# Performance work log

Measured on AMD Instinct MI355X. Metric: run time of the kernel, lower is better.

## Reference

```python
import jax, jax.numpy as jnp
import numpy as np

N, E, G = 100000, 1600000, 1000
F_IN, H, C = 16, 64, 2
EPS = 1e-5


def setup_inputs() -> dict:
    key = jax.random.key(0)
    ks = jax.random.split(key, 8)

    def lin(k, i, o):
        return (jax.random.normal(k, (i, o), jnp.float32) / np.float32(np.sqrt(i)))

    return {
        "x": jax.random.normal(ks[0], (N, F_IN), jnp.float32),
        "edge_index": jax.random.randint(ks[1], (2, E), 0, N),
        "batch": jnp.sort(jax.random.randint(ks[2], (N,), 0, G)),
        # GraphNorm params: weight=1, bias=0, mean_scale(alpha)=1 (PyG init)
        "gn0_w": jnp.ones(F_IN, jnp.float32), "gn0_b": jnp.zeros(F_IN, jnp.float32), "gn0_a": jnp.ones(F_IN, jnp.float32),
        "W1": lin(ks[3], F_IN, H), "b1": jnp.zeros(H, jnp.float32),
        "gn1_w": jnp.ones(H, jnp.float32), "gn1_b": jnp.zeros(H, jnp.float32), "gn1_a": jnp.ones(H, jnp.float32),
        "W2": lin(ks[4], H, H), "b2": jnp.zeros(H, jnp.float32),
        "gn2_w": jnp.ones(H, jnp.float32), "gn2_b": jnp.zeros(H, jnp.float32), "gn2_a": jnp.ones(H, jnp.float32),
        "W3": lin(ks[5], H, H), "b3": jnp.zeros(H, jnp.float32),
        "Wd": lin(ks[6], H, H), "bd": jnp.zeros(H, jnp.float32),
        "Wo": lin(ks[7], H, C), "bo": jnp.zeros(C, jnp.float32),
    }


def _graph_norm(x, batch, w, b, a):
    counts = jnp.maximum(jax.ops.segment_sum(jnp.ones(x.shape[0], x.dtype), batch, G), 1.0)[:, None]
    mean = jax.ops.segment_sum(x, batch, G) / counts          # [G, F]
    out = x - a * mean[batch]
    var = jax.ops.segment_sum(out * out, batch, G) / counts   # [G, F]
    return w * (out * jax.lax.rsqrt(var + EPS)[batch]) + b


def _gcn_conv(x, W, b, src, dst):
    # PyG GCNConv: D^{-1/2}(A+I)D^{-1/2} X W + b, deg includes self-loop
    h = x @ W                                                  # [N, out]
    deg = jax.ops.segment_sum(jnp.ones(src.shape[0], x.dtype), dst, N) + 1.0
    dinv = jax.lax.rsqrt(deg)
    msg = h[src] * (dinv[src] * dinv[dst])[:, None]            # [E, out]
    agg = jax.ops.segment_sum(msg, dst, N) + h / deg[:, None]  # self-loop term: 1/deg
    return agg + b


def reference(x, edge_index, batch, gn0_w, gn0_b, gn0_a, W1, b1,
              gn1_w, gn1_b, gn1_a, W2, b2, gn2_w, gn2_b, gn2_a,
              W3, b3, Wd, bd, Wo, bo):
    src, dst = edge_index[0], edge_index[1]
    x = _graph_norm(x, batch, gn0_w, gn0_b, gn0_a)
    x = jax.nn.relu(_gcn_conv(x, W1, b1, src, dst))
    x = _graph_norm(x, batch, gn1_w, gn1_b, gn1_a)
    x = jax.nn.relu(_gcn_conv(x, W2, b2, src, dst))
    x = _graph_norm(x, batch, gn2_w, gn2_b, gn2_a)
    x = jax.nn.relu(_gcn_conv(x, W3, b3, src, dst))
    counts = jnp.maximum(jax.ops.segment_sum(jnp.ones(N, x.dtype), batch, G), 1.0)
    pooled = jax.ops.segment_sum(x, batch, G) / counts[:, None]  # global_mean_pool [G, H]
    # dropout p=0.5 is identity in eval mode
    h = jax.nn.relu(pooled @ Wd + bd)
    logits = h @ Wo + bo
    return jax.nn.softmax(logits, axis=1)
```

## Files before the change

kernel.cpp:

```cpp
#include <hip/hip_runtime.h>
#include <hip/hip_fp16.h>
#include <math.h>

#define NB_NODES 100000
#define NB_EDGES 1600000
#define NB_GRAPHS 1000
#define CAP 232
#define NBLK1 400
#define CHUNK 4000
#define NBUCK 391
#define BCAP 4608
constexpr float GN_EPS = 1e-5f;

__global__ __launch_bounds__(256) void k1_hist(const int* __restrict__ dst,
    int* __restrict__ hist, const int* __restrict__ batch, int* __restrict__ gstart) {
    __shared__ int h[NBUCK];
    int tid = threadIdx.x;
    for (int i = tid; i < NBUCK; i += 256) h[i] = 0;
    if (blockIdx.x < 4) {
        int g = blockIdx.x * 256 + tid;
        if (g <= NB_GRAPHS) {
            int lo = 0, hi = NB_NODES;
            while (lo < hi) {
                int mid = (lo + hi) >> 1;
                if (batch[mid] < g) lo = mid + 1; else hi = mid;
            }
            gstart[g] = lo;
        }
    }
    __syncthreads();
    int base = blockIdx.x * CHUNK;
    for (int i = tid; i < CHUNK; i += 256) atomicAdd(&h[dst[base + i] >> 8], 1);
    __syncthreads();
    for (int i = tid; i < NBUCK; i += 256) hist[blockIdx.x * NBUCK + i] = h[i];
}

__global__ __launch_bounds__(512) void k2a_scan(int* __restrict__ hist,
                                                int* __restrict__ total) {
    __shared__ int s[512];
    int b = blockIdx.x;
    int tid = threadIdx.x;
    int v = (tid < NBLK1) ? hist[tid * NBUCK + b] : 0;
    s[tid] = v;
    __syncthreads();
    for (int o = 1; o < 512; o <<= 1) {
        int t = (tid >= o) ? s[tid - o] : 0;
        __syncthreads();
        s[tid] += t;
        __syncthreads();
    }
    if (tid < NBLK1) hist[tid * NBUCK + b] = s[tid] - v;
    if (tid == 511) total[b] = s[511];
}

__global__ __launch_bounds__(256) void k3_scatter(const int* __restrict__ ei,
    const int* __restrict__ hist, const int* __restrict__ total,
    unsigned int* __restrict__ ebuf) {
    __shared__ int cur[NBUCK];
    __shared__ int sc[256];
    int tid = threadIdx.x;
    int e0 = 2 * tid, e1 = 2 * tid + 1;
    int v0 = (e0 < NBUCK) ? total[e0] : 0;
    int v1 = (e1 < NBUCK) ? total[e1] : 0;
    int own = v0 + v1;
    sc[tid] = own;
    __syncthreads();
    for (int o = 1; o < 256; o <<= 1) {
        int t = (tid >= o) ? sc[tid - o] : 0;
        __syncthreads();
        sc[tid] += t;
        __syncthreads();
    }
    int pre = sc[tid] - own;
    if (e0 < NBUCK) cur[e0] = pre + hist[blockIdx.x * NBUCK + e0];
    if (e1 < NBUCK) cur[e1] = pre + v0 + hist[blockIdx.x * NBUCK + e1];
    __syncthreads();
    int eb = blockIdx.x * CHUNK;
    for (int i = tid; i < CHUNK; i += 256) {
        int e = eb + i;
        int sidx = ei[e];
        int d = ei[NB_EDGES + e];
        int pos = atomicAdd(&cur[d >> 8], 1);
        ebuf[pos] = (unsigned int)sidx | ((unsigned int)(d & 255) << 24);
    }
}

__global__ __launch_bounds__(256) void k4_fine(const unsigned int* __restrict__ ebuf,
    const int* __restrict__ total, int* __restrict__ csr_src, int* __restrict__ rowptr,
    float* __restrict__ dinv) {
    __shared__ int arena[2 * BCAP + 768];
    unsigned int* epk = (unsigned int*)arena;
    int* outb  = arena + BCAP;
    int* cnt   = arena + 2 * BCAP;
    int* sbuf  = arena + 2 * BCAP + 256;
    int* cur2  = arena + 2 * BCAP + 512;
    int* bases = arena + 2 * BCAP;
    int b = blockIdx.x;
    int tid = threadIdx.x;
    int e0 = 2 * tid, e1 = 2 * tid + 1;
    int v0 = (e0 < NBUCK) ? total[e0] : 0;
    int v1 = (e1 < NBUCK) ? total[e1] : 0;
    int own = v0 + v1;
    cur2[tid] = own;
    __syncthreads();
    for (int o = 1; o < 256; o <<= 1) {
        int t = (tid >= o) ? cur2[tid - o] : 0;
        __syncthreads();
        cur2[tid] += t;
        __syncthreads();
    }
    int pre = cur2[tid] - own;
    if (e0 < NBUCK) bases[e0] = pre;
    if (e1 < NBUCK) bases[e1] = pre + v0;
    if (tid == 0) bases[NBUCK] = NB_EDGES;
    __syncthreads();
    int eb = bases[b], ee = bases[b + 1];
    __syncthreads();
    int m = ee - eb;
    if (m > BCAP) m = BCAP;
    for (int i = tid; i < m; i += 256) epk[i] = ebuf[eb + i];
    cnt[tid] = 0;
    __syncthreads();
    for (int i = tid; i < m; i += 256) atomicAdd(&cnt[epk[i] >> 24], 1);
    __syncthreads();
    int c = cnt[tid];
    sbuf[tid] = c;
    __syncthreads();
    for (int o = 1; o < 256; o <<= 1) {
        int t = (tid >= o) ? sbuf[tid - o] : 0;
        __syncthreads();
        sbuf[tid] += t;
        __syncthreads();
    }
    int off = sbuf[tid] - c;
    cur2[tid] = off;
    __syncthreads();
    for (int i = tid; i < m; i += 256) {
        unsigned int p = epk[i];
        int r = atomicAdd(&cur2[p >> 24], 1);
        outb[r] = (int)(p & 0x00FFFFFFu);
    }
    __syncthreads();
    for (int i = tid; i < m; i += 256) csr_src[eb + i] = outb[i];
    int node = b * 256 + tid;
    if (node < NB_NODES) {
        rowptr[node] = eb + off;
        dinv[node] = rsqrtf((float)(c + 1));
    }
    if (b == 0 && tid == 0) rowptr[NB_NODES] = NB_EDGES;
}

union HU {
    uint4 u;
    __half2 h[4];
};

__device__ __forceinline__ void pkacc(__half2* a, uint4 v) {
    HU x; x.u = v;
    a[0] = __hadd2(a[0], x.h[0]);
    a[1] = __hadd2(a[1], x.h[1]);
    a[2] = __hadd2(a[2], x.h[2]);
    a[3] = __hadd2(a[3], x.h[3]);
}

__device__ __forceinline__ __half2 shxor_h2(__half2 v, int m) {
    union { __half2 h; int i; } u;
    u.h = v;
    u.i = __shfl_xor(u.i, m, 64);
    return u.h;
}

__global__ __launch_bounds__(256) void aggregate_h_k(const __half* __restrict__ hs,
    const int* __restrict__ rowptr, const int* __restrict__ csr_src,
    const float* __restrict__ dinv, const float* __restrict__ bias,
    __half* __restrict__ out) {
    const uint4* hsv = (const uint4*)hs;
    int wv = blockIdx.x * 4 + (threadIdx.x >> 6);
    int lane = threadIdx.x & 63;
    int f8 = lane & 7;
    int e8 = lane >> 3;
    int n0 = __builtin_amdgcn_readfirstlane(wv * 4);
    int r0 = rowptr[n0], r1 = rowptr[n0 + 1], r2 = rowptr[n0 + 2];
    int r3 = rowptr[n0 + 3], r4 = rowptr[n0 + 4];
    int d0 = r1 - r0, d1 = r2 - r1, d2 = r3 - r2, d3 = r4 - r3;
    const uint4 Z = {0u, 0u, 0u, 0u};
    int idx0 = (lane < d0) ? csr_src[r0 + lane] : -1;
    int idx1 = (lane < d1) ? csr_src[r1 + lane] : -1;
    int idx2 = (lane < d2) ? csr_src[r2 + lane] : -1;
    int idx3 = (lane < d3) ? csr_src[r3 + lane] : -1;
    uint4 self = Z;
    if (e8 < 4) self = hsv[(size_t)(n0 + e8) * 8 + f8];
    uint4 gA[8];
#pragma unroll
    for (int b = 0; b < 4; b++) {
        int u = __shfl(idx0, b * 8 + e8, 64);
        gA[b] = Z;
        if (u >= 0) gA[b] = hsv[(size_t)u * 8 + f8];
        int v = __shfl(idx1, b * 8 + e8, 64);
        gA[4 + b] = Z;
        if (v >= 0) gA[4 + b] = hsv[(size_t)v * 8 + f8];
    }
    __half2 acc0[4], acc1[4], acc2[4], acc3[4];
    __half2 z2{__half(0.f), __half(0.f)};
    acc0[0] = acc0[1] = acc0[2] = acc0[3] = z2;
    acc1[0] = acc1[1] = acc1[2] = acc1[3] = z2;
    acc2[0] = acc2[1] = acc2[2] = acc2[3] = z2;
    acc3[0] = acc3[1] = acc3[2] = acc3[3] = z2;
    if (e8 == 0) pkacc(acc0, self);
    if (e8 == 1) pkacc(acc1, self);
    if (e8 == 2) pkacc(acc2, self);
    if (e8 == 3) pkacc(acc3, self);
    uint4 gB[8];
#pragma unroll
    for (int b = 0; b < 4; b++) {
        int u = __shfl(idx2, b * 8 + e8, 64);
        gB[b] = Z;
        if (u >= 0) gB[b] = hsv[(size_t)u * 8 + f8];
        int v = __shfl(idx3, b * 8 + e8, 64);
        gB[4 + b] = Z;
        if (v >= 0) gB[4 + b] = hsv[(size_t)v * 8 + f8];
    }
#pragma unroll
    for (int b = 0; b < 4; b++) { pkacc(acc0, gA[b]); pkacc(acc1, gA[4 + b]); }
#pragma unroll
    for (int b = 0; b < 4; b++) { pkacc(acc2, gB[b]); pkacc(acc3, gB[4 + b]); }
    int tb0 = (d0 + 7) >> 3, tb1 = (d1 + 7) >> 3;
    int tb2 = (d2 + 7) >> 3, tb3 = (d3 + 7) >> 3;
    for (int b = 4; b < tb0 && b < 8; b++) {
        int u = __shfl(idx0, b * 8 + e8, 64);
        if (u >= 0) pkacc(acc0, hsv[(size_t)u * 8 + f8]);
    }
    for (int b = 4; b < tb1 && b < 8; b++) {
        int u = __shfl(idx1, b * 8 + e8, 64);
        if (u >= 0) pkacc(acc1, hsv[(size_t)u * 8 + f8]);
    }
    for (int b = 4; b < tb2 && b < 8; b++) {
        int u = __shfl(idx2, b * 8 + e8, 64);
        if (u >= 0) pkacc(acc2, hsv[(size_t)u * 8 + f8]);
    }
    for (int b = 4; b < tb3 && b < 8; b++) {
        int u = __shfl(idx3, b * 8 + e8, 64);
        if (u >= 0) pkacc(acc3, hsv[(size_t)u * 8 + f8]);
    }
    for (int b = 8; b < tb0; b++) {
        int j = r0 + b * 8 + e8;
        if (j < r1) pkacc(acc0, hsv[(size_t)csr_src[j] * 8 + f8]);
    }
    for (int b = 8; b < tb1; b++) {
        int j = r1 + b * 8 + e8;
        if (j < r2) pkacc(acc1, hsv[(size_t)csr_src[j] * 8 + f8]);
    }
    for (int b = 8; b < tb2; b++) {
        int j = r2 + b * 8 + e8;
        if (j < r3) pkacc(acc2, hsv[(size_t)csr_src[j] * 8 + f8]);
    }
    for (int b = 8; b < tb3; b++) {
        int j = r3 + b * 8 + e8;
        if (j < r4) pkacc(acc3, hsv[(size_t)csr_src[j] * 8 + f8]);
    }
#pragma unroll
    for (int c = 0; c < 4; c++) {
        __half2 t0 = acc0[c];
        t0 = __hadd2(t0, shxor_h2(t0, 8));
        t0 = __hadd2(t0, shxor_h2(t0, 16));
        t0 = __hadd2(t0, shxor_h2(t0, 32));
        acc0[c] = t0;
        __half2 t1 = acc1[c];
        t1 = __hadd2(t1, shxor_h2(t1, 8));
        t1 = __hadd2(t1, shxor_h2(t1, 16));
        t1 = __hadd2(t1, shxor_h2(t1, 32));
        acc1[c] = t1;
        __half2 t2 = acc2[c];
        t2 = __hadd2(t2, shxor_h2(t2, 8));
        t2 = __hadd2(t2, shxor_h2(t2, 16));
        t2 = __hadd2(t2, shxor_h2(t2, 32));
        acc2[c] = t2;
        __half2 t3 = acc3[c];
        t3 = __hadd2(t3, shxor_h2(t3, 8));
        t3 = __hadd2(t3, shxor_h2(t3, 16));
        t3 = __hadd2(t3, shxor_h2(t3, 32));
        acc3[c] = t3;
    }
    if (e8 < 4) {
        int node = n0 + e8;
        const __half2* acc = (e8 == 0) ? acc0 : (e8 == 1) ? acc1 : (e8 == 2) ? acc2 : acc3;
        float dn = dinv[node];
        const float4* b4 = (const float4*)bias;
        float4 blo = b4[f8 * 2], bhi = b4[f8 * 2 + 1];
        float2 f0 = __half22float2(acc[0]);
        float2 f1 = __half22float2(acc[1]);
        float2 f2 = __half22float2(acc[2]);
        float2 f3 = __half22float2(acc[3]);
        float r[8];
        r[0] = fmaf(f0.x, dn, blo.x); r[1] = fmaf(f0.y, dn, blo.y);
        r[2] = fmaf(f1.x, dn, blo.z); r[3] = fmaf(f1.y, dn, blo.w);
        r[4] = fmaf(f2.x, dn, bhi.x); r[5] = fmaf(f2.y, dn, bhi.y);
        r[6] = fmaf(f3.x, dn, bhi.z); r[7] = fmaf(f3.y, dn, bhi.w);
#pragma unroll
        for (int c = 0; c < 8; c++) r[c] = r[c] > 0.f ? r[c] : 0.f;
        HU o;
        o.h[0] = __floats2half2_rn(r[0], r[1]);
        o.h[1] = __floats2half2_rn(r[2], r[3]);
        o.h[2] = __floats2half2_rn(r[4], r[5]);
        o.h[3] = __floats2half2_rn(r[6], r[7]);
        ((uint4*)out)[(size_t)node * 8 + f8] = o.u;
    }
}

__global__ __launch_bounds__(512) void normlin_k(const __half* __restrict__ A,
    const int* __restrict__ gstart, const float* __restrict__ gw,
    const float* __restrict__ gb, const float* __restrict__ ga,
    const float* __restrict__ W, const float* __restrict__ dinv,
    __half* __restrict__ out) {
    __shared__ float sW[64 * 64];
    __shared__ float red[512], red2[512];
    __shared__ float sam[64], ssc[64];
    __shared__ float srow[8 * 64];
    int tid = threadIdx.x, lane = tid & 63, wid = tid >> 6;
    int g = blockIdx.x;
    int s = gstart[g], e = gstart[g + 1], cnt = e - s;
    float cntf = (float)(cnt > 1 ? cnt : 1);
    for (int i = tid; i < 64 * 64; i += 512) sW[i] = W[i];
    float sum = 0.f, sq = 0.f;
    for (int i = s + wid; i < e; i += 8) {
        float v = __half2float(A[(size_t)i * 64 + lane]);
        sum += v;
        sq = fmaf(v, v, sq);
    }
    red[tid] = sum; red2[tid] = sq;
    __syncthreads();
    for (int st = 4; st > 0; st >>= 1) {
        if (wid < st) { red[tid] += red[tid + st * 64]; red2[tid] += red2[tid + st * 64]; }
        __syncthreads();
    }
    if (tid < 64) {
        float m = red[tid] / cntf, q = red2[tid] / cntf;
        float am = ga[tid] * m;
        float var = q - 2.f * am * m + am * am;
        sam[tid] = am;
        ssc[tid] = gw[tid] * rsqrtf(var + GN_EPS);
    }
    __syncthreads();
    float am = sam[lane], sc = ssc[lane], bb = gb[lane];
    for (int i = s + wid; i < e; i += 8) {
        float nv = (__half2float(A[(size_t)i * 64 + lane]) - am) * sc + bb;
        srow[wid * 64 + lane] = nv;
        float acc = 0.f;
#pragma unroll
        for (int k = 0; k < 64; k++) acc = fmaf(srow[wid * 64 + k], sW[k * 64 + lane], acc);
        out[(size_t)i * 64 + lane] = __float2half(acc * dinv[i]);
    }
}

__device__ __forceinline__ void l0_body(float* rows, int cnt, int s,
    const float* __restrict__ x, const float* __restrict__ gw,
    const float* __restrict__ gb, const float* __restrict__ ga,
    const float* sW, const float* __restrict__ dinv, __half* __restrict__ hs_out,
    float* red, float* red2, float* sstat, float* sscale, int tid) {
    int f = tid & 15, r = tid >> 4;
    int lane = tid & 63, wid = tid >> 6;
    float cntf = (float)(cnt > 1 ? cnt : 1);
    float sum = 0.f, sq = 0.f;
    for (int i = r; i < cnt; i += 32) {
        float v = x[(size_t)(s + i) * 16 + f];
        rows[i * 16 + f] = v;
        sum += v;
        sq = fmaf(v, v, sq);
    }
    red[tid] = sum; red2[tid] = sq;
    __syncthreads();
    for (int st = 16; st > 0; st >>= 1) {
        if (r < st) { red[tid] += red[tid + st * 16]; red2[tid] += red2[tid + st * 16]; }
        __syncthreads();
    }
    if (tid < 16) {
        float m = red[tid] / cntf, q = red2[tid] / cntf;
        float am = ga[tid] * m;
        sstat[tid] = am;
        sscale[tid] = gw[tid] * rsqrtf(q - 2.f * am * m + am * am + GN_EPS);
    }
    __syncthreads();
    float am = sstat[f], sc = sscale[f], bb = gb[f];
    for (int i = r; i < cnt; i += 32) rows[i * 16 + f] = (rows[i * 16 + f] - am) * sc + bb;
    __syncthreads();
    for (int i = wid; i < cnt; i += 8) {
        float acc = 0.f;
#pragma unroll
        for (int k = 0; k < 16; k++) acc = fmaf(rows[i * 16 + k], sW[k * 64 + lane], acc);
        hs_out[(size_t)(s + i) * 64 + lane] = __float2half(acc * dinv[s + i]);
    }
}

__global__ __launch_bounds__(512) void layer0_k(const float* __restrict__ x,
    const int* __restrict__ gstart, const float* __restrict__ gw,
    const float* __restrict__ gb, const float* __restrict__ ga,
    const float* __restrict__ W, const float* __restrict__ dinv,
    __half* __restrict__ hs_out, float* __restrict__ spill16) {
    __shared__ float sRows[CAP * 16];
    __shared__ float sW[16 * 64];
    __shared__ float red[512], red2[512];
    __shared__ float sstat[16], sscale[16];
    int tid = threadIdx.x;
    int g = blockIdx.x;
    int s = gstart[g], e = gstart[g + 1], cnt = e - s;
    for (int i = tid; i < 16 * 64; i += 512) sW[i] = W[i];
    __syncthreads();
    if (cnt <= CAP)
        l0_body(sRows, cnt, s, x, gw, gb, ga, sW, dinv, hs_out, red, red2, sstat, sscale, tid);
    else
        l0_body(spill16 + (size_t)s * 16, cnt, s, x, gw, gb, ga, sW, dinv, hs_out, red, red2, sstat, sscale, tid);
}

__global__ void pool_head_k(const __half* __restrict__ x, const int* __restrict__ gstart,
                            const float* __restrict__ Wd, const float* __restrict__ bd,
                            const float* __restrict__ Wo, const float* __restrict__ bo,
                            float* __restrict__ out) {
    __shared__ float red[256];
    __shared__ float sp[64];
    __shared__ float sh[64];
    __shared__ float sl[2];
    int g = blockIdx.x;
    int s = gstart[g], e = gstart[g + 1];
    int cnt = e - s;
    float cntf = (float)(cnt > 1 ? cnt : 1);
    int tid = threadIdx.x;
    int f = tid & 63, r = tid >> 6;
    float sum = 0.f;
    for (int i = s + r; i < e; i += 4) sum += __half2float(x[(size_t)i * 64 + f]);
    red[tid] = sum;
    __syncthreads();
    for (int st = 2; st > 0; st >>= 1) {
        if (r < st) red[tid] += red[tid + st * 64];
        __syncthreads();
    }
    if (tid < 64) sp[tid] = red[tid] / cntf;
    __syncthreads();
    if (tid < 64) {
        float acc = bd[tid];
        for (int k = 0; k < 64; k++) acc = fmaf(sp[k], Wd[k * 64 + tid], acc);
        sh[tid] = acc > 0.f ? acc : 0.f;
    }
    __syncthreads();
    if (tid < 2) {
        float l = bo[tid];
        for (int k = 0; k < 64; k++) l = fmaf(sh[k], Wo[k * 2 + tid], l);
        sl[tid] = l;
    }
    __syncthreads();
    if (tid < 2) {
        float m = fmaxf(sl[0], sl[1]);
        float e0 = expf(sl[0] - m), e1 = expf(sl[1] - m);
        out[g * 2 + tid] = (tid == 0 ? e0 : e1) / (e0 + e1);
    }
}

extern "C" void kernel_launch(void* const* d_in, const int* in_sizes, int n_in,
                              void* d_out, int out_size, void* d_ws, size_t ws_size,
                              hipStream_t stream) {
    const float* x    = (const float*)d_in[0];
    const int* ei     = (const int*)d_in[1];
    const int* batch  = (const int*)d_in[2];
    const float* gn0w = (const float*)d_in[3];
    const float* gn0b = (const float*)d_in[4];
    const float* gn0a = (const float*)d_in[5];
    const float* W1   = (const float*)d_in[6];
    const float* b1   = (const float*)d_in[7];
    const float* gn1w = (const float*)d_in[8];
    const float* gn1b = (const float*)d_in[9];
    const float* gn1a = (const float*)d_in[10];
    const float* W2   = (const float*)d_in[11];
    const float* b2   = (const float*)d_in[12];
    const float* gn2w = (const float*)d_in[13];
    const float* gn2b = (const float*)d_in[14];
    const float* gn2a = (const float*)d_in[15];
    const float* W3   = (const float*)d_in[16];
    const float* b3   = (const float*)d_in[17];
    const float* Wd   = (const float*)d_in[18];
    const float* bd   = (const float*)d_in[19];
    const float* Wo   = (const float*)d_in[20];
    const float* bo   = (const float*)d_in[21];

    char* p = (char*)d_ws;
    auto alloc = [&](size_t bytes) -> void* {
        void* r = (void*)p;
        p += (bytes + 255) & ~(size_t)255;
        return r;
    };
    __half* A        = (__half*)alloc((size_t)NB_NODES * 64 * 2);
    __half* B        = (__half*)alloc((size_t)NB_NODES * 64 * 2);
    int* rowptr      = (int*)alloc((size_t)(NB_NODES + 1) * 4);
    unsigned* ebuf   = (unsigned*)alloc((size_t)NB_EDGES * 4);
    int* csr_src     = (int*)alloc((size_t)NB_EDGES * 4);
    int* hist        = (int*)alloc((size_t)NBLK1 * NBUCK * 4);
    int* total       = (int*)alloc((size_t)NBUCK * 4);
    float* dinv      = (float*)alloc((size_t)NB_NODES * 4);
    int* gstart      = (int*)alloc((size_t)(NB_GRAPHS + 1) * 4);
    float* spill16   = (float*)alloc((size_t)NB_NODES * 16 * 4);

    k1_hist<<<NBLK1, 256, 0, stream>>>(ei + NB_EDGES, hist, batch, gstart);
    k2a_scan<<<NBUCK, 512, 0, stream>>>(hist, total);
    k3_scatter<<<NBLK1, 256, 0, stream>>>(ei, hist, total, ebuf);
    k4_fine<<<NBUCK, 256, 0, stream>>>(ebuf, total, csr_src, rowptr, dinv);

    layer0_k<<<NB_GRAPHS, 512, 0, stream>>>(x, gstart, gn0w, gn0b, gn0a, W1, dinv, B, spill16);
    aggregate_h_k<<<6250, 256, 0, stream>>>(B, rowptr, csr_src, dinv, b1, A);
    normlin_k<<<NB_GRAPHS, 512, 0, stream>>>(A, gstart, gn1w, gn1b, gn1a, W2, dinv, B);
    aggregate_h_k<<<6250, 256, 0, stream>>>(B, rowptr, csr_src, dinv, b2, A);
    normlin_k<<<NB_GRAPHS, 512, 0, stream>>>(A, gstart, gn2w, gn2b, gn2a, W3, dinv, B);
    aggregate_h_k<<<6250, 256, 0, stream>>>(B, rowptr, csr_src, dinv, b3, A);
    pool_head_k<<<NB_GRAPHS, 256, 0, stream>>>(A, gstart, Wd, bd, Wo, bo, (float*)d_out);
}
```

Before: 325.2 us.

## Fuse GCN aggregation with per-graph GraphNorm+linear and final pooling head

```diff
diff --git a/kernel.cpp b/kernel.cpp
--- a/kernel.cpp
+++ b/kernel.cpp
@@ -170,18 +170,15 @@
     return u.h;
 }
 
-__global__ __launch_bounds__(256) void aggregate_h_k(const __half* __restrict__ hs,
+__device__ __forceinline__ int agg4_core(const uint4* __restrict__ hsv,
     const int* __restrict__ rowptr, const int* __restrict__ csr_src,
     const float* __restrict__ dinv, const float* __restrict__ bias,
-    __half* __restrict__ out) {
-    const uint4* hsv = (const uint4*)hs;
-    int wv = blockIdx.x * 4 + (threadIdx.x >> 6);
-    int lane = threadIdx.x & 63;
-    int f8 = lane & 7;
-    int e8 = lane >> 3;
-    int n0 = __builtin_amdgcn_readfirstlane(wv * 4);
-    int r0 = rowptr[n0], r1 = rowptr[n0 + 1], r2 = rowptr[n0 + 2];
-    int r3 = rowptr[n0 + 3], r4 = rowptr[n0 + 4];
+    int n0, int e, int lane, int f8, int e8, float r[8]) {
+    int i2 = n0 + 2 < e ? n0 + 2 : e;
+    int i3 = n0 + 3 < e ? n0 + 3 : e;
+    int i4 = n0 + 4 < e ? n0 + 4 : e;
+    int r0 = rowptr[n0], r1 = rowptr[n0 + 1], r2 = rowptr[i2];
+    int r3 = rowptr[i3], r4 = rowptr[i4];
     int d0 = r1 - r0, d1 = r2 - r1, d2 = r3 - r2, d3 = r4 - r3;
     const uint4 Z = {0u, 0u, 0u, 0u};
     int idx0 = (lane < d0) ? csr_src[r0 + lane] : -1;
@@ -189,17 +186,7 @@
     int idx2 = (lane < d2) ? csr_src[r2 + lane] : -1;
     int idx3 = (lane < d3) ? csr_src[r3 + lane] : -1;
     uint4 self = Z;
-    if (e8 < 4) self = hsv[(size_t)(n0 + e8) * 8 + f8];
-    uint4 gA[8];
-#pragma unroll
-    for (int b = 0; b < 4; b++) {
-        int u = __shfl(idx0, b * 8 + e8, 64);
-        gA[b] = Z;
-        if (u >= 0) gA[b] = hsv[(size_t)u * 8 + f8];
-        int v = __shfl(idx1, b * 8 + e8, 64);
-        gA[4 + b] = Z;
-        if (v >= 0) gA[4 + b] = hsv[(size_t)v * 8 + f8];
-    }
+    if (e8 < 4 && n0 + e8 < e) self = hsv[(size_t)(n0 + e8) * 8 + f8];
     __half2 acc0[4], acc1[4], acc2[4], acc3[4];
     __half2 z2{__half(0.f), __half(0.f)};
     acc0[0] = acc0[1] = acc0[2] = acc0[3] = z2;
@@ -210,20 +197,29 @@
     if (e8 == 1) pkacc(acc1, self);
     if (e8 == 2) pkacc(acc2, self);
     if (e8 == 3) pkacc(acc3, self);
-    uint4 gB[8];
+    uint4 g[8];
+#pragma unroll
+    for (int b = 0; b < 4; b++) {
+        int u = __shfl(idx0, b * 8 + e8, 64);
+        g[b] = Z;
+        if (u >= 0) g[b] = hsv[(size_t)u * 8 + f8];
+        int v = __shfl(idx1, b * 8 + e8, 64);
+        g[4 + b] = Z;
+        if (v >= 0) g[4 + b] = hsv[(size_t)v * 8 + f8];
+    }
+#pragma unroll
+    for (int b = 0; b < 4; b++) { pkacc(acc0, g[b]); pkacc(acc1, g[4 + b]); }
 #pragma unroll
     for (int b = 0; b < 4; b++) {
         int u = __shfl(idx2, b * 8 + e8, 64);
-        gB[b] = Z;
-        if (u >= 0) gB[b] = hsv[(size_t)u * 8 + f8];
+        g[b] = Z;
+        if (u >= 0) g[b] = hsv[(size_t)u * 8 + f8];
         int v = __shfl(idx3, b * 8 + e8, 64);
-        gB[4 + b] = Z;
-        if (v >= 0) gB[4 + b] = hsv[(size_t)v * 8 + f8];
-    }
-#pragma unroll
-    for (int b = 0; b < 4; b++) { pkacc(acc0, gA[b]); pkacc(acc1, gA[4 + b]); }
-#pragma unroll
-    for (int b = 0; b < 4; b++) { pkacc(acc2, gB[b]); pkacc(acc3, gB[4 + b]); }
+        g[4 + b] = Z;
+        if (v >= 0) g[4 + b] = hsv[(size_t)v * 8 + f8];
+    }
+#pragma unroll
+    for (int b = 0; b < 4; b++) { pkacc(acc2, g[b]); pkacc(acc3, g[4 + b]); }
     int tb0 = (d0 + 7) >> 3, tb1 = (d1 + 7) >> 3;
     int tb2 = (d2 + 7) >> 3, tb3 = (d3 + 7) >> 3;
     for (int b = 4; b < tb0 && b < 8; b++) {
@@ -281,74 +277,172 @@
         t3 = __hadd2(t3, shxor_h2(t3, 32));
         acc3[c] = t3;
     }
-    if (e8 < 4) {
-        int node = n0 + e8;
-        const __half2* acc = (e8 == 0) ? acc0 : (e8 == 1) ? acc1 : (e8 == 2) ? acc2 : acc3;
-        float dn = dinv[node];
-        const float4* b4 = (const float4*)bias;
-        float4 blo = b4[f8 * 2], bhi = b4[f8 * 2 + 1];
-        float2 f0 = __half22float2(acc[0]);
-        float2 f1 = __half22float2(acc[1]);
-        float2 f2 = __half22float2(acc[2]);
-        float2 f3 = __half22float2(acc[3]);
-        float r[8];
-        r[0] = fmaf(f0.x, dn, blo.x); r[1] = fmaf(f0.y, dn, blo.y);
-        r[2] = fmaf(f1.x, dn, blo.z); r[3] = fmaf(f1.y, dn, blo.w);
-        r[4] = fmaf(f2.x, dn, bhi.x); r[5] = fmaf(f2.y, dn, bhi.y);
-        r[6] = fmaf(f3.x, dn, bhi.z); r[7] = fmaf(f3.y, dn, bhi.w);
-#pragma unroll
-        for (int c = 0; c < 8; c++) r[c] = r[c] > 0.f ? r[c] : 0.f;
-        HU o;
-        o.h[0] = __floats2half2_rn(r[0], r[1]);
-        o.h[1] = __floats2half2_rn(r[2], r[3]);
-        o.h[2] = __floats2half2_rn(r[4], r[5]);
-        o.h[3] = __floats2half2_rn(r[6], r[7]);
-        ((uint4*)out)[(size_t)node * 8 + f8] = o.u;
-    }
-}
-
-__global__ __launch_bounds__(512) void normlin_k(const __half* __restrict__ A,
-    const int* __restrict__ gstart, const float* __restrict__ gw,
+    if (e8 >= 4) return -1;
+    int node = n0 + e8;
+    if (node >= e) return -1;
+    const __half2* acc = (e8 == 0) ? acc0 : (e8 == 1) ? acc1 : (e8 == 2) ? acc2 : acc3;
+    float dn = dinv[node];
+    const float4* b4 = (const float4*)bias;
+    float4 blo = b4[f8 * 2], bhi = b4[f8 * 2 + 1];
+    float2 f0 = __half22float2(acc[0]);
+    float2 f1 = __half22float2(acc[1]);
+    float2 f2 = __half22float2(acc[2]);
+    float2 f3 = __half22float2(acc[3]);
+    r[0] = fmaf(f0.x, dn, blo.x); r[1] = fmaf(f0.y, dn, blo.y);
+    r[2] = fmaf(f1.x, dn, blo.z); r[3] = fmaf(f1.y, dn, blo.w);
+    r[4] = fmaf(f2.x, dn, bhi.x); r[5] = fmaf(f2.y, dn, bhi.y);
+    r[6] = fmaf(f3.x, dn, bhi.z); r[7] = fmaf(f3.y, dn, bhi.w);
+#pragma unroll
+    for (int c = 0; c < 8; c++) r[c] = r[c] > 0.f ? r[c] : 0.f;
+    return node;
+}
+
+__device__ __forceinline__ void aggnorm_body(__half* rows, int s, int cnt, int e,
+    const uint4* __restrict__ hsv, const int* __restrict__ rowptr,
+    const int* __restrict__ csr_src, const float* __restrict__ dinv,
+    const float* __restrict__ bias, const float* __restrict__ gw,
     const float* __restrict__ gb, const float* __restrict__ ga,
-    const float* __restrict__ W, const float* __restrict__ dinv,
-    __half* __restrict__ out) {
-    __shared__ float sW[64 * 64];
-    __shared__ float red[512], red2[512];
-    __shared__ float sam[64], ssc[64];
-    __shared__ float srow[8 * 64];
+    const float* __restrict__ W, __half* __restrict__ out,
+    float* red, float* red2, float* sam, float* ssc, float* srow) {
     int tid = threadIdx.x, lane = tid & 63, wid = tid >> 6;
-    int g = blockIdx.x;
-    int s = gstart[g], e = gstart[g + 1], cnt = e - s;
+    int f8 = lane & 7, e8 = lane >> 3;
+    int passes = (cnt + 15) >> 4;
+    for (int p = 0; p < passes; ++p) {
+        int n0 = __builtin_amdgcn_readfirstlane(s + p * 16 + wid * 4);
+        if (n0 < e) {
+            float r[8];
+            int node = agg4_core(hsv, rowptr, csr_src, dinv, bias, n0, e, lane, f8, e8, r);
+            if (node >= 0) {
+                HU o;
+                o.h[0] = __floats2half2_rn(r[0], r[1]);
+                o.h[1] = __floats2half2_rn(r[2], r[3]);
+                o.h[2] = __floats2half2_rn(r[4], r[5]);
+                o.h[3] = __floats2half2_rn(r[6], r[7]);
+                ((uint4*)rows)[(size_t)(node - s) * 8 + f8] = o.u;
+            }
+        }
+    }
+    __syncthreads();
     float cntf = (float)(cnt > 1 ? cnt : 1);
-    for (int i = tid; i < 64 * 64; i += 512) sW[i] = W[i];
     float sum = 0.f, sq = 0.f;
-    for (int i = s + wid; i < e; i += 8) {
-        float v = __half2float(A[(size_t)i * 64 + lane]);
+    for (int i = wid; i < cnt; i += 4) {
+        float v = __half2float(rows[(size_t)i * 64 + lane]);
         sum += v;
         sq = fmaf(v, v, sq);
     }
     red[tid] = sum; red2[tid] = sq;
     __syncthreads();
-    for (int st = 4; st > 0; st >>= 1) {
+    for (int st = 2; st > 0; st >>= 1) {
         if (wid < st) { red[tid] += red[tid + st * 64]; red2[tid] += red2[tid + st * 64]; }
         __syncthreads();
     }
     if (tid < 64) {
         float m = red[tid] / cntf, q = red2[tid] / cntf;
         float am = ga[tid] * m;
-        float var = q - 2.f * am * m + am * am;
         sam[tid] = am;
-        ssc[tid] = gw[tid] * rsqrtf(var + GN_EPS);
-    }
-    __syncthreads();
+        ssc[tid] = gw[tid] * rsqrtf(q - 2.f * am * m + am * am + GN_EPS);
+    }
+    __syncthreads();
+    float wcol[64];
+#pragma unroll
+    for (int k = 0; k < 64; k++) wcol[k] = W[k * 64 + lane];
     float am = sam[lane], sc = ssc[lane], bb = gb[lane];
-    for (int i = s + wid; i < e; i += 8) {
-        float nv = (__half2float(A[(size_t)i * 64 + lane]) - am) * sc + bb;
+    for (int i = wid; i < cnt; i += 4) {
+        float nv = (__half2float(rows[(size_t)i * 64 + lane]) - am) * sc + bb;
         srow[wid * 64 + lane] = nv;
         float acc = 0.f;
 #pragma unroll
-        for (int k = 0; k < 64; k++) acc = fmaf(srow[wid * 64 + k], sW[k * 64 + lane], acc);
-        out[(size_t)i * 64 + lane] = __float2half(acc * dinv[i]);
+        for (int k = 0; k < 64; k++) acc = fmaf(srow[wid * 64 + k], wcol[k], acc);
+        out[(size_t)(s + i) * 64 + lane] = __float2half(acc * dinv[s + i]);
+    }
+}
+
+__global__ __launch_bounds__(256, 4) void fused_aggnorm_k(
+    const __half* __restrict__ hs_in, const int* __restrict__ gstart,
+    const int* __restrict__ rowptr, const int* __restrict__ csr_src,
+    const float* __restrict__ dinv, const float* __restrict__ bias,
+    const float* __restrict__ gw, const float* __restrict__ gb,
+    const float* __restrict__ ga, const float* __restrict__ W,
+    __half* __restrict__ out, __half* __restrict__ spill) {
+    __shared__ alignas(16) __half sA[CAP * 64];
+    __shared__ float red[256], red2[256];
+    __shared__ float sam[64], ssc[64];
+    __shared__ float srow[4 * 64];
+    int g = blockIdx.x;
+    int s = gstart[g], e = gstart[g + 1], cnt = e - s;
+    const uint4* hsv = (const uint4*)hs_in;
+    if (cnt <= CAP)
+        aggnorm_body(sA, s, cnt, e, hsv, rowptr, csr_src, dinv, bias,
+                     gw, gb, ga, W, out, red, red2, sam, ssc, srow);
+    else
+        aggnorm_body(spill + (size_t)s * 64, s, cnt, e, hsv, rowptr, csr_src, dinv, bias,
+                     gw, gb, ga, W, out, red, red2, sam, ssc, srow);
+}
+
+__global__ __launch_bounds__(256, 4) void fused_aggpool_k(
+    const __half* __restrict__ hs_in, const int* __restrict__ gstart,
+    const int* __restrict__ rowptr, const int* __restrict__ csr_src,
+    const float* __restrict__ dinv, const float* __restrict__ bias,
+    const float* __restrict__ Wd, const float* __restrict__ bd,
+    const float* __restrict__ Wo, const float* __restrict__ bo,
+    float* __restrict__ out) {
+    __shared__ float wpart[4 * 64];
+    __shared__ float sp[64];
+    __shared__ float sh[64];
+    __shared__ float sl[2];
+    int tid = threadIdx.x, lane = tid & 63, wid = tid >> 6;
+    int f8 = lane & 7, e8 = lane >> 3;
+    int g = blockIdx.x;
+    int s = gstart[g], e = gstart[g + 1], cnt = e - s;
+    const uint4* hsv = (const uint4*)hs_in;
+    float pacc[8];
+#pragma unroll
+    for (int j = 0; j < 8; j++) pacc[j] = 0.f;
+    int passes = (cnt + 15) >> 4;
+    for (int p = 0; p < passes; ++p) {
+        int n0 = __builtin_amdgcn_readfirstlane(s + p * 16 + wid * 4);
+        if (n0 < e) {
+            float r[8];
+            int node = agg4_core(hsv, rowptr, csr_src, dinv, bias, n0, e, lane, f8, e8, r);
+            if (node >= 0) {
+#pragma unroll
+                for (int j = 0; j < 8; j++) pacc[j] += r[j];
+            }
+        }
+    }
+#pragma unroll
+    for (int j = 0; j < 8; j++) {
+        float v = pacc[j];
+        v += __shfl_xor(v, 8, 64);
+        v += __shfl_xor(v, 16, 64);
+        v += __shfl_xor(v, 32, 64);
+        pacc[j] = v;
+    }
+    if (lane < 8) {
+#pragma unroll
+        for (int j = 0; j < 8; j++) wpart[wid * 64 + lane * 8 + j] = pacc[j];
+    }
+    __syncthreads();
+    float cntf = (float)(cnt > 1 ? cnt : 1);
+    if (tid < 64)
+        sp[tid] = (wpart[tid] + wpart[64 + tid] + wpart[128 + tid] + wpart[192 + tid]) / cntf;
+    __syncthreads();
+    if (tid < 64) {
+        float acc = bd[tid];
+        for (int k = 0; k < 64; k++) acc = fmaf(sp[k], Wd[k * 64 + tid], acc);
+        sh[tid] = acc > 0.f ? acc : 0.f;
+    }
+    __syncthreads();
+    if (tid < 2) {
+        float l = bo[tid];
+        for (int k = 0; k < 64; k++) l = fmaf(sh[k], Wo[k * 2 + tid], l);
+        sl[tid] = l;
+    }
+    __syncthreads();
+    if (tid < 2) {
+        float m = fmaxf(sl[0], sl[1]);
+        float e0 = expf(sl[0] - m), e1 = expf(sl[1] - m);
+        out[g * 2 + tid] = (tid == 0 ? e0 : e1) / (e0 + e1);
     }
 }
 
@@ -409,49 +503,6 @@
         l0_body(sRows, cnt, s, x, gw, gb, ga, sW, dinv, hs_out, red, red2, sstat, sscale, tid);
     else
         l0_body(spill16 + (size_t)s * 16, cnt, s, x, gw, gb, ga, sW, dinv, hs_out, red, red2, sstat, sscale, tid);
-}
-
-__global__ void pool_head_k(const __half* __restrict__ x, const int* __restrict__ gstart,
-                            const float* __restrict__ Wd, const float* __restrict__ bd,
-                            const float* __restrict__ Wo, const float* __restrict__ bo,
-                            float* __restrict__ out) {
-    __shared__ float red[256];
-    __shared__ float sp[64];
-    __shared__ float sh[64];
-    __shared__ float sl[2];
-    int g = blockIdx.x;
-    int s = gstart[g], e = gstart[g + 1];
-    int cnt = e - s;
-    float cntf = (float)(cnt > 1 ? cnt : 1);
-    int tid = threadIdx.x;
-    int f = tid & 63, r = tid >> 6;
-    float sum = 0.f;
-    for (int i = s + r; i < e; i += 4) sum += __half2float(x[(size_t)i * 64 + f]);
-    red[tid] = sum;
-    __syncthreads();
-    for (int st = 2; st > 0; st >>= 1) {
-        if (r < st) red[tid] += red[tid + st * 64];
-        __syncthreads();
-    }
-    if (tid < 64) sp[tid] = red[tid] / cntf;
-    __syncthreads();
-    if (tid < 64) {
-        float acc = bd[tid];
-        for (int k = 0; k < 64; k++) acc = fmaf(sp[k], Wd[k * 64 + tid], acc);
-        sh[tid] = acc > 0.f ? acc : 0.f;
-    }
-    __syncthreads();
-    if (tid < 2) {
-        float l = bo[tid];
-        for (int k = 0; k < 64; k++) l = fmaf(sh[k], Wo[k * 2 + tid], l);
-        sl[tid] = l;
-    }
-    __syncthreads();
-    if (tid < 2) {
-        float m = fmaxf(sl[0], sl[1]);
-        float e0 = expf(sl[0] - m), e1 = expf(sl[1] - m);
-        out[g * 2 + tid] = (tid == 0 ? e0 : e1) / (e0 + e1);
-    }
 }
 
 extern "C" void kernel_launch(void* const* d_in, const int* in_sizes, int n_in,
@@ -496,6 +547,7 @@
     float* dinv      = (float*)alloc((size_t)NB_NODES * 4);
     int* gstart      = (int*)alloc((size_t)(NB_GRAPHS + 1) * 4);
     float* spill16   = (float*)alloc((size_t)NB_NODES * 16 * 4);
+    __half* spillH   = (__half*)alloc((size_t)NB_NODES * 64 * 2);
 
     k1_hist<<<NBLK1, 256, 0, stream>>>(ei + NB_EDGES, hist, batch, gstart);
     k2a_scan<<<NBUCK, 512, 0, stream>>>(hist, total);
@@ -503,10 +555,10 @@
     k4_fine<<<NBUCK, 256, 0, stream>>>(ebuf, total, csr_src, rowptr, dinv);
 
     layer0_k<<<NB_GRAPHS, 512, 0, stream>>>(x, gstart, gn0w, gn0b, gn0a, W1, dinv, B, spill16);
-    aggregate_h_k<<<6250, 256, 0, stream>>>(B, rowptr, csr_src, dinv, b1, A);
-    normlin_k<<<NB_GRAPHS, 512, 0, stream>>>(A, gstart, gn1w, gn1b, gn1a, W2, dinv, B);
-    aggregate_h_k<<<6250, 256, 0, stream>>>(B, rowptr, csr_src, dinv, b2, A);
-    normlin_k<<<NB_GRAPHS, 512, 0, stream>>>(A, gstart, gn2w, gn2b, gn2a, W3, dinv, B);
-    aggregate_h_k<<<6250, 256, 0, stream>>>(B, rowptr, csr_src, dinv, b3, A);
-    pool_head_k<<<NB_GRAPHS, 256, 0, stream>>>(A, gstart, Wd, bd, Wo, bo, (float*)d_out);
-}
+    fused_aggnorm_k<<<NB_GRAPHS, 256, 0, stream>>>(B, gstart, rowptr, csr_src, dinv,
+                                                   b1, gn1w, gn1b, gn1a, W2, A, spillH);
+    fused_aggnorm_k<<<NB_GRAPHS, 256, 0, stream>>>(A, gstart, rowptr, csr_src, dinv,
+                                                   b2, gn2w, gn2b, gn2a, W3, B, spillH);
+    fused_aggpool_k<<<NB_GRAPHS, 256, 0, stream>>>(B, gstart, rowptr, csr_src, dinv,
+                                                   b3, Wd, bd, Wo, bo, (float*)d_out);
+}
```

After: 298.0 us. -8.4%, faster.

## Fuse GCN aggregation with GraphNorm+linear per graph using chunked feature layout

Applied to the files above, without the earlier changes.

```diff
diff --git a/kernel.cpp b/kernel.cpp
--- a/kernel.cpp
+++ b/kernel.cpp
@@ -6,6 +6,8 @@
 #define NB_EDGES 1600000
 #define NB_GRAPHS 1000
 #define CAP 232
+#define NCH 4
+#define ECAP 2048
 #define NBLK1 400
 #define CHUNK 4000
 #define NBUCK 391
@@ -170,185 +172,179 @@
     return u.h;
 }
 
-__global__ __launch_bounds__(256) void aggregate_h_k(const __half* __restrict__ hs,
+template<bool LDSE>
+__device__ __forceinline__ void gather_rows(__half* rows, int s, int cnt, int eb,
+    const uint4* __restrict__ hsv, const int* __restrict__ rowptr,
+    const int* __restrict__ csr_src, const int* eidx, int tid) {
+    const int lane = tid & 63, wid = tid >> 6;
+    const int f2 = lane & 1, es = (lane >> 1) & 7, n2 = lane >> 4;
+    uint4* rows_u4 = (uint4*)rows;
+    const __half2 z2{__half(0.f), __half(0.f)};
+    int passes = (cnt + 15) >> 4;
+    for (int c = 0; c < NCH; ++c) {
+        const size_t cbase = (size_t)c * NB_NODES;
+        for (int p = 0; p < passes; ++p) {
+            int ln = p * 16 + wid * 4 + n2;
+            int rb = 0, d = 0;
+            if (ln < cnt) { rb = rowptr[s + ln]; d = rowptr[s + ln + 1] - rb; }
+            __half2 acc[4] = {z2, z2, z2, z2};
+            if (es == 0 && ln < cnt) {
+                pkacc(acc, hsv[(cbase + (size_t)(s + ln)) * 2 + f2]);
+            }
+#pragma unroll
+            for (int b = 0; b < 4; ++b) {
+                int t = b * 8 + es;
+                if (t < d) {
+                    int u = LDSE ? eidx[rb - eb + t] : csr_src[rb + t];
+                    pkacc(acc, hsv[(cbase + (size_t)u) * 2 + f2]);
+                }
+            }
+            int dm = d;
+            dm = max(dm, __shfl_xor(dm, 16, 64));
+            dm = max(dm, __shfl_xor(dm, 32, 64));
+            for (int b = 4; b * 8 < dm; ++b) {
+                int t = b * 8 + es;
+                if (t < d) {
+                    int u = LDSE ? eidx[rb - eb + t] : csr_src[rb + t];
+                    pkacc(acc, hsv[(cbase + (size_t)u) * 2 + f2]);
+                }
+            }
+#pragma unroll
+            for (int j = 0; j < 4; ++j) {
+                acc[j] = __hadd2(acc[j], shxor_h2(acc[j], 2));
+                acc[j] = __hadd2(acc[j], shxor_h2(acc[j], 4));
+                acc[j] = __hadd2(acc[j], shxor_h2(acc[j], 8));
+            }
+            if (es == 0 && ln < cnt) {
+                HU o;
+                o.h[0] = acc[0]; o.h[1] = acc[1]; o.h[2] = acc[2]; o.h[3] = acc[3];
+                rows_u4[(size_t)ln * 8 + c * 2 + f2] = o.u;
+            }
+        }
+    }
+}
+
+__global__ __launch_bounds__(256, 4) void fused_aggnorm_k(
+    const __half* __restrict__ hs_in, const int* __restrict__ gstart,
     const int* __restrict__ rowptr, const int* __restrict__ csr_src,
     const float* __restrict__ dinv, const float* __restrict__ bias,
-    __half* __restrict__ out) {
-    const uint4* hsv = (const uint4*)hs;
-    int wv = blockIdx.x * 4 + (threadIdx.x >> 6);
-    int lane = threadIdx.x & 63;
-    int f8 = lane & 7;
-    int e8 = lane >> 3;
-    int n0 = __builtin_amdgcn_readfirstlane(wv * 4);
-    int r0 = rowptr[n0], r1 = rowptr[n0 + 1], r2 = rowptr[n0 + 2];
-    int r3 = rowptr[n0 + 3], r4 = rowptr[n0 + 4];
-    int d0 = r1 - r0, d1 = r2 - r1, d2 = r3 - r2, d3 = r4 - r3;
-    const uint4 Z = {0u, 0u, 0u, 0u};
-    int idx0 = (lane < d0) ? csr_src[r0 + lane] : -1;
-    int idx1 = (lane < d1) ? csr_src[r1 + lane] : -1;
-    int idx2 = (lane < d2) ? csr_src[r2 + lane] : -1;
-    int idx3 = (lane < d3) ? csr_src[r3 + lane] : -1;
-    uint4 self = Z;
-    if (e8 < 4) self = hsv[(size_t)(n0 + e8) * 8 + f8];
-    uint4 gA[8];
-#pragma unroll
-    for (int b = 0; b < 4; b++) {
-        int u = __shfl(idx0, b * 8 + e8, 64);
-        gA[b] = Z;
-        if (u >= 0) gA[b] = hsv[(size_t)u * 8 + f8];
-        int v = __shfl(idx1, b * 8 + e8, 64);
-        gA[4 + b] = Z;
-        if (v >= 0) gA[4 + b] = hsv[(size_t)v * 8 + f8];
-    }
-    __half2 acc0[4], acc1[4], acc2[4], acc3[4];
-    __half2 z2{__half(0.f), __half(0.f)};
-    acc0[0] = acc0[1] = acc0[2] = acc0[3] = z2;
-    acc1[0] = acc1[1] = acc1[2] = acc1[3] = z2;
-    acc2[0] = acc2[1] = acc2[2] = acc2[3] = z2;
-    acc3[0] = acc3[1] = acc3[2] = acc3[3] = z2;
-    if (e8 == 0) pkacc(acc0, self);
-    if (e8 == 1) pkacc(acc1, self);
-    if (e8 == 2) pkacc(acc2, self);
-    if (e8 == 3) pkacc(acc3, self);
-    uint4 gB[8];
-#pragma unroll
-    for (int b = 0; b < 4; b++) {
-        int u = __shfl(idx2, b * 8 + e8, 64);
-        gB[b] = Z;
-        if (u >= 0) gB[b] = hsv[(size_t)u * 8 + f8];
-        int v = __shfl(idx3, b * 8 + e8, 64);
-        gB[4 + b] = Z;
-        if (v >= 0) gB[4 + b] = hsv[(size_t)v * 8 + f8];
-    }
-#pragma unroll
-    for (int b = 0; b < 4; b++) { pkacc(acc0, gA[b]); pkacc(acc1, gA[4 + b]); }
-#pragma unroll
-    for (int b = 0; b < 4; b++) { pkacc(acc2, gB[b]); pkacc(acc3, gB[4 + b]); }
-    int tb0 = (d0 + 7) >> 3, tb1 = (d1 + 7) >> 3;
-    int tb2 = (d2 + 7) >> 3, tb3 = (d3 + 7) >> 3;
-    for (int b = 4; b < tb0 && b < 8; b++) {
-        int u = __shfl(idx0, b * 8 + e8, 64);
-        if (u >= 0) pkacc(acc0, hsv[(size_t)u * 8 + f8]);
-    }
-    for (int b = 4; b < tb1 && b < 8; b++) {
-        int u = __shfl(idx1, b * 8 + e8, 64);
-        if (u >= 0) pkacc(acc1, hsv[(size_t)u * 8 + f8]);
-    }
-    for (int b = 4; b < tb2 && b < 8; b++) {
-        int u = __shfl(idx2, b * 8 + e8, 64);
-        if (u >= 0) pkacc(acc2, hsv[(size_t)u * 8 + f8]);
-    }
-    for (int b = 4; b < tb3 && b < 8; b++) {
-        int u = __shfl(idx3, b * 8 + e8, 64);
-        if (u >= 0) pkacc(acc3, hsv[(size_t)u * 8 + f8]);
-    }
-    for (int b = 8; b < tb0; b++) {
-        int j = r0 + b * 8 + e8;
-        if (j < r1) pkacc(acc0, hsv[(size_t)csr_src[j] * 8 + f8]);
-    }
-    for (int b = 8; b < tb1; b++) {
-        int j = r1 + b * 8 + e8;
-        if (j < r2) pkacc(acc1, hsv[(size_t)csr_src[j] * 8 + f8]);
-    }
-    for (int b = 8; b < tb2; b++) {
-        int j = r2 + b * 8 + e8;
-        if (j < r3) pkacc(acc2, hsv[(size_t)csr_src[j] * 8 + f8]);
-    }
-    for (int b = 8; b < tb3; b++) {
-        int j = r3 + b * 8 + e8;
-        if (j < r4) pkacc(acc3, hsv[(size_t)csr_src[j] * 8 + f8]);
-    }
-#pragma unroll
-    for (int c = 0; c < 4; c++) {
-        __half2 t0 = acc0[c];
-        t0 = __hadd2(t0, shxor_h2(t0, 8));
-        t0 = __hadd2(t0, shxor_h2(t0, 16));
-        t0 = __hadd2(t0, shxor_h2(t0, 32));
-        acc0[c] = t0;
-        __half2 t1 = acc1[c];
-        t1 = __hadd2(t1, shxor_h2(t1, 8));
-        t1 = __hadd2(t1, shxor_h2(t1, 16));
-        t1 = __hadd2(t1, shxor_h2(t1, 32));
-        acc1[c] = t1;
-        __half2 t2 = acc2[c];
-        t2 = __hadd2(t2, shxor_h2(t2, 8));
-        t2 = __hadd2(t2, shxor_h2(t2, 16));
-        t2 = __hadd2(t2, shxor_h2(t2, 32));
-        acc2[c] = t2;
-        __half2 t3 = acc3[c];
-        t3 = __hadd2(t3, shxor_h2(t3, 8));
-        t3 = __hadd2(t3, shxor_h2(t3, 16));
-        t3 = __hadd2(t3, shxor_h2(t3, 32));
-        acc3[c] = t3;
-    }
-    if (e8 < 4) {
-        int node = n0 + e8;
-        const __half2* acc = (e8 == 0) ? acc0 : (e8 == 1) ? acc1 : (e8 == 2) ? acc2 : acc3;
-        float dn = dinv[node];
-        const float4* b4 = (const float4*)bias;
-        float4 blo = b4[f8 * 2], bhi = b4[f8 * 2 + 1];
-        float2 f0 = __half22float2(acc[0]);
-        float2 f1 = __half22float2(acc[1]);
-        float2 f2 = __half22float2(acc[2]);
-        float2 f3 = __half22float2(acc[3]);
-        float r[8];
-        r[0] = fmaf(f0.x, dn, blo.x); r[1] = fmaf(f0.y, dn, blo.y);
-        r[2] = fmaf(f1.x, dn, blo.z); r[3] = fmaf(f1.y, dn, blo.w);
-        r[4] = fmaf(f2.x, dn, bhi.x); r[5] = fmaf(f2.y, dn, bhi.y);
-        r[6] = fmaf(f3.x, dn, bhi.z); r[7] = fmaf(f3.y, dn, bhi.w);
-#pragma unroll
-        for (int c = 0; c < 8; c++) r[c] = r[c] > 0.f ? r[c] : 0.f;
-        HU o;
-        o.h[0] = __floats2half2_rn(r[0], r[1]);
-        o.h[1] = __floats2half2_rn(r[2], r[3]);
-        o.h[2] = __floats2half2_rn(r[4], r[5]);
-        o.h[3] = __floats2half2_rn(r[6], r[7]);
-        ((uint4*)out)[(size_t)node * 8 + f8] = o.u;
-    }
-}
-
-__global__ __launch_bounds__(512) void normlin_k(const __half* __restrict__ A,
-    const int* __restrict__ gstart, const float* __restrict__ gw,
-    const float* __restrict__ gb, const float* __restrict__ ga,
-    const float* __restrict__ W, const float* __restrict__ dinv,
-    __half* __restrict__ out) {
-    __shared__ float sW[64 * 64];
-    __shared__ float red[512], red2[512];
+    const float* __restrict__ gw, const float* __restrict__ gb,
+    const float* __restrict__ ga, const float* __restrict__ W,
+    __half* __restrict__ out, __half* __restrict__ spill) {
+    __shared__ alignas(16) __half sA[CAP * 64];
+    __shared__ int arena[ECAP];
     __shared__ float sam[64], ssc[64];
-    __shared__ float srow[8 * 64];
     int tid = threadIdx.x, lane = tid & 63, wid = tid >> 6;
     int g = blockIdx.x;
     int s = gstart[g], e = gstart[g + 1], cnt = e - s;
+    int eb = rowptr[s], m = rowptr[e] - eb;
+    const uint4* hsv = (const uint4*)hs_in;
+    __half* rows = (cnt <= CAP) ? sA : (spill + (size_t)s * 64);
+    bool lds_e = (m <= ECAP);
+    if (lds_e) for (int i = tid; i < m; i += 256) arena[i] = csr_src[eb + i];
+    __syncthreads();
+    if (lds_e) gather_rows<true >(rows, s, cnt, eb, hsv, rowptr, csr_src, arena, tid);
+    else       gather_rows<false>(rows, s, cnt, eb, hsv, rowptr, csr_src, arena, tid);
+    __syncthreads();
+    float* red  = (float*)arena;
+    float* red2 = red + 256;
+    float* srow = red2 + 256;
     float cntf = (float)(cnt > 1 ? cnt : 1);
-    for (int i = tid; i < 64 * 64; i += 512) sW[i] = W[i];
+    float bb = bias[lane];
     float sum = 0.f, sq = 0.f;
-    for (int i = s + wid; i < e; i += 8) {
-        float v = __half2float(A[(size_t)i * 64 + lane]);
-        sum += v;
-        sq = fmaf(v, v, sq);
+    for (int i = wid; i < cnt; i += 4) {
+        float h = fmaf(__half2float(rows[(size_t)i * 64 + lane]), dinv[s + i], bb);
+        h = h > 0.f ? h : 0.f;
+        sum += h;
+        sq = fmaf(h, h, sq);
     }
     red[tid] = sum; red2[tid] = sq;
     __syncthreads();
-    for (int st = 4; st > 0; st >>= 1) {
+    for (int st = 2; st > 0; st >>= 1) {
         if (wid < st) { red[tid] += red[tid + st * 64]; red2[tid] += red2[tid + st * 64]; }
         __syncthreads();
     }
     if (tid < 64) {
-        float m = red[tid] / cntf, q = red2[tid] / cntf;
-        float am = ga[tid] * m;
-        float var = q - 2.f * am * m + am * am;
+        float mn = red[tid] / cntf, q = red2[tid] / cntf;
+        float am = ga[tid] * mn;
         sam[tid] = am;
-        ssc[tid] = gw[tid] * rsqrtf(var + GN_EPS);
-    }
-    __syncthreads();
-    float am = sam[lane], sc = ssc[lane], bb = gb[lane];
-    for (int i = s + wid; i < e; i += 8) {
-        float nv = (__half2float(A[(size_t)i * 64 + lane]) - am) * sc + bb;
+        ssc[tid] = gw[tid] * rsqrtf(q - 2.f * am * mn + am * am + GN_EPS);
+    }
+    __syncthreads();
+    float wcol[64];
+#pragma unroll
+    for (int k = 0; k < 64; k++) wcol[k] = W[k * 64 + lane];
+    float am = sam[lane], sc = ssc[lane], bbg = gb[lane];
+    int co = lane >> 4, fo = lane & 15;
+    for (int i = wid; i < cnt; i += 4) {
+        float dn = dinv[s + i];
+        float h = fmaf(__half2float(rows[(size_t)i * 64 + lane]), dn, bb);
+        h = h > 0.f ? h : 0.f;
+        float nv = (h - am) * sc + bbg;
         srow[wid * 64 + lane] = nv;
-        float acc = 0.f;
+        float a = 0.f;
 #pragma unroll
-        for (int k = 0; k < 64; k++) acc = fmaf(srow[wid * 64 + k], sW[k * 64 + lane], acc);
-        out[(size_t)i * 64 + lane] = __float2half(acc * dinv[i]);
+        for (int k = 0; k < 64; k++) a = fmaf(srow[wid * 64 + k], wcol[k], a);
+        out[((size_t)co * NB_NODES + (s + i)) * 16 + fo] = __float2half(a * dn);
+    }
+}
+
+__global__ __launch_bounds__(256, 4) void fused_aggpool_k(
+    const __half* __restrict__ hs_in, const int* __restrict__ gstart,
+    const int* __restrict__ rowptr, const int* __restrict__ csr_src,
+    const float* __restrict__ dinv, const float* __restrict__ bias,
+    const float* __restrict__ Wd, const float* __restrict__ bd,
+    const float* __restrict__ Wo, const float* __restrict__ bo,
+    float* __restrict__ out, __half* __restrict__ spill) {
+    __shared__ alignas(16) __half sA[CAP * 64];
+    __shared__ int arena[ECAP];
+    __shared__ float sp[64];
+    __shared__ float sh[64];
+    __shared__ float sl[2];
+    int tid = threadIdx.x, lane = tid & 63, wid = tid >> 6;
+    int g = blockIdx.x;
+    int s = gstart[g], e = gstart[g + 1], cnt = e - s;
+    int eb = rowptr[s], m = rowptr[e] - eb;
+    const uint4* hsv = (const uint4*)hs_in;
+    __half* rows = (cnt <= CAP) ? sA : (spill + (size_t)s * 64);
+    bool lds_e = (m <= ECAP);
+    if (lds_e) for (int i = tid; i < m; i += 256) arena[i] = csr_src[eb + i];
+    __syncthreads();
+    if (lds_e) gather_rows<true >(rows, s, cnt, eb, hsv, rowptr, csr_src, arena, tid);
+    else       gather_rows<false>(rows, s, cnt, eb, hsv, rowptr, csr_src, arena, tid);
+    __syncthreads();
+    float* red = (float*)arena;
+    float cntf = (float)(cnt > 1 ? cnt : 1);
+    float bb = bias[lane];
+    float sum = 0.f;
+    for (int i = wid; i < cnt; i += 4) {
+        float h = fmaf(__half2float(rows[(size_t)i * 64 + lane]), dinv[s + i], bb);
+        sum += (h > 0.f ? h : 0.f);
+    }
+    red[tid] = sum;
+    __syncthreads();
+    for (int st = 2; st > 0; st >>= 1) {
+        if (wid < st) red[tid] += red[tid + st * 64];
+        __syncthreads();
+    }
+    if (tid < 64) sp[tid] = red[tid] / cntf;
+    __syncthreads();
+    if (tid < 64) {
+        float acc = bd[tid];
+        for (int k = 0; k < 64; k++) acc = fmaf(sp[k], Wd[k * 64 + tid], acc);
+        sh[tid] = acc > 0.f ? acc : 0.f;
+    }
+    __syncthreads();
+    if (tid < 2) {
+        float l = bo[tid];
+        for (int k = 0; k < 64; k++) l = fmaf(sh[k], Wo[k * 2 + tid], l);
+        sl[tid] = l;
+    }
+    __syncthreads();
+    if (tid < 2) {
+        float mx = fmaxf(sl[0], sl[1]);
+        float e0 = expf(sl[0] - mx), e1 = expf(sl[1] - mx);
+        out[g * 2 + tid] = (tid == 0 ? e0 : e1) / (e0 + e1);
     }
 }
 
@@ -383,11 +379,12 @@
     float am = sstat[f], sc = sscale[f], bb = gb[f];
     for (int i = r; i < cnt; i += 32) rows[i * 16 + f] = (rows[i * 16 + f] - am) * sc + bb;
     __syncthreads();
+    int co = lane >> 4, fo = lane & 15;
     for (int i = wid; i < cnt; i += 8) {
         float acc = 0.f;
 #pragma unroll
         for (int k = 0; k < 16; k++) acc = fmaf(rows[i * 16 + k], sW[k * 64 + lane], acc);
-        hs_out[(size_t)(s + i) * 64 + lane] = __float2half(acc * dinv[s + i]);
+        hs_out[((size_t)co * NB_NODES + (s + i)) * 16 + fo] = __float2half(acc * dinv[s + i]);
     }
 }
 
@@ -409,49 +406,6 @@
         l0_body(sRows, cnt, s, x, gw, gb, ga, sW, dinv, hs_out, red, red2, sstat, sscale, tid);
     else
         l0_body(spill16 + (size_t)s * 16, cnt, s, x, gw, gb, ga, sW, dinv, hs_out, red, red2, sstat, sscale, tid);
-}
-
-__global__ void pool_head_k(const __half* __restrict__ x, const int* __restrict__ gstart,
-                            const float* __restrict__ Wd, const float* __restrict__ bd,
-                            const float* __restrict__ Wo, const float* __restrict__ bo,
-                            float* __restrict__ out) {
-    __shared__ float red[256];
-    __shared__ float sp[64];
-    __shared__ float sh[64];
-    __shared__ float sl[2];
-    int g = blockIdx.x;
-    int s = gstart[g], e = gstart[g + 1];
-    int cnt = e - s;
-    float cntf = (float)(cnt > 1 ? cnt : 1);
-    int tid = threadIdx.x;
-    int f = tid & 63, r = tid >> 6;
-    float sum = 0.f;
-    for (int i = s + r; i < e; i += 4) sum += __half2float(x[(size_t)i * 64 + f]);
-    red[tid] = sum;
-    __syncthreads();
-    for (int st = 2; st > 0; st >>= 1) {
-        if (r < st) red[tid] += red[tid + st * 64];
-        __syncthreads();
-    }
-    if (tid < 64) sp[tid] = red[tid] / cntf;
-    __syncthreads();
-    if (tid < 64) {
-        float acc = bd[tid];
-        for (int k = 0; k < 64; k++) acc = fmaf(sp[k], Wd[k * 64 + tid], acc);
-        sh[tid] = acc > 0.f ? acc : 0.f;
-    }
-    __syncthreads();
-    if (tid < 2) {
-        float l = bo[tid];
-        for (int k = 0; k < 64; k++) l = fmaf(sh[k], Wo[k * 2 + tid], l);
-        sl[tid] = l;
-    }
-    __syncthreads();
-    if (tid < 2) {
-        float m = fmaxf(sl[0], sl[1]);
-        float e0 = expf(sl[0] - m), e1 = expf(sl[1] - m);
-        out[g * 2 + tid] = (tid == 0 ? e0 : e1) / (e0 + e1);
-    }
 }
 
 extern "C" void kernel_launch(void* const* d_in, const int* in_sizes, int n_in,
@@ -496,6 +450,7 @@
     float* dinv      = (float*)alloc((size_t)NB_NODES * 4);
     int* gstart      = (int*)alloc((size_t)(NB_GRAPHS + 1) * 4);
     float* spill16   = (float*)alloc((size_t)NB_NODES * 16 * 4);
+    __half* spillH   = (__half*)alloc((size_t)NB_NODES * 64 * 2);
 
     k1_hist<<<NBLK1, 256, 0, stream>>>(ei + NB_EDGES, hist, batch, gstart);
     k2a_scan<<<NBUCK, 512, 0, stream>>>(hist, total);
@@ -503,10 +458,10 @@
     k4_fine<<<NBUCK, 256, 0, stream>>>(ebuf, total, csr_src, rowptr, dinv);
 
     layer0_k<<<NB_GRAPHS, 512, 0, stream>>>(x, gstart, gn0w, gn0b, gn0a, W1, dinv, B, spill16);
-    aggregate_h_k<<<6250, 256, 0, stream>>>(B, rowptr, csr_src, dinv, b1, A);
-    normlin_k<<<NB_GRAPHS, 512, 0, stream>>>(A, gstart, gn1w, gn1b, gn1a, W2, dinv, B);
-    aggregate_h_k<<<6250, 256, 0, stream>>>(B, rowptr, csr_src, dinv, b2, A);
-    normlin_k<<<NB_GRAPHS, 512, 0, stream>>>(A, gstart, gn2w, gn2b, gn2a, W3, dinv, B);
-    aggregate_h_k<<<6250, 256, 0, stream>>>(B, rowptr, csr_src, dinv, b3, A);
-    pool_head_k<<<NB_GRAPHS, 256, 0, stream>>>(A, gstart, Wd, bd, Wo, bo, (float*)d_out);
-}
+    fused_aggnorm_k<<<NB_GRAPHS, 256, 0, stream>>>(B, gstart, rowptr, csr_src, dinv,
+                                                   b1, gn1w, gn1b, gn1a, W2, A, spillH);
+    fused_aggnorm_k<<<NB_GRAPHS, 256, 0, stream>>>(A, gstart, rowptr, csr_src, dinv,
+                                                   b2, gn2w, gn2b, gn2a, W3, B, spillH);
+    fused_aggpool_k<<<NB_GRAPHS, 256, 0, stream>>>(B, gstart, rowptr, csr_src, dinv,
+                                                   b3, Wd, bd, Wo, bo, (float*)d_out, spillH);
+}
```

New measurement: 473.1 us. 1.46x slower.
